# Kernel optimization log

Hardware: AMD Instinct MI355X
Metric: run time of the kernel (lower is better)

## Reference

```python
import jax, jax.numpy as jnp
import numpy as np

E = 65536
C = 128            # hidden_channels
SPH = 128          # sphere_channels
EC = 128           # edge_channels
LMAX = 3
MMAX = 2
S = 1 + 2 * LMAX   # 7
DEG_FULL = [2 * l + 1 for l in range(1, LMAX + 1)]          # [3,5,7], sum=15
DEG_RED = [min(2 * l + 1, 2 * MMAX + 1) for l in range(1, LMAX + 1)]  # [3,5,5]
D_FULL = sum(DEG_FULL)


def setup_inputs() -> dict:
    key = jax.random.key(0)
    ks = jax.random.split(key, 10)
    return {
        "attn_output": jax.random.normal(ks[0], (E, S * C), jnp.float32),
        "t_ij": jax.random.normal(ks[1], (E, EC), jnp.float32),
        "h_j": jax.random.normal(ks[2], (E, SPH), jnp.float32),
        "X_j": jax.random.normal(ks[3], (E, D_FULL, SPH), jnp.float32),
        "rl_ij": jax.random.normal(ks[4], (E, D_FULL), jnp.float32),
        # learned params
        "W_rs_w": jax.random.normal(ks[5], (S * C, EC), jnp.float32) * 0.02,
        "W_rs_b": jnp.zeros((S * C,), jnp.float32),
        "gamma_w": jax.random.normal(ks[6], (S * C, SPH), jnp.float32) * 0.02,
        "gamma_b": jnp.zeros((S * C,), jnp.float32),
        "xj_w": jax.random.normal(ks[7], (C, SPH), jnp.float32) * 0.02,
    }


def reference(attn_output, t_ij, h_j, X_j, rl_ij, W_rs_w, W_rs_b, gamma_w, gamma_b, xj_w):
    # Eq. 6: combined = attn + (t_ij W_rs) * SiLU(gamma(h_j))
    t_bias = (t_ij @ W_rs_w.T + W_rs_b) * jax.nn.silu(h_j @ gamma_w.T + gamma_b)
    combined = attn_output + t_bias              # [E, S*C]
    # split(C, dim=-1) == reshape to [E, S, C]
    o = combined.reshape(-1, S, C)
    out_scalar = jax.nn.silu(o[:, 0])[:, None, :]  # [E,1,C]
    # project neighbour features: [E, D_FULL, SPH] -> [E, D_FULL, C]
    Xp = jnp.einsum('eds,cs->edc', X_j, xj_w)
    offs = np.concatenate([[0], np.cumsum(DEG_FULL)])
    out_degrees = [out_scalar]
    for i in range(LMAX):
        m = DEG_RED[i]
        s0 = int(offs[i])
        Xl = Xp[:, s0:s0 + m, :]                  # [E, m, C]
        rl = rl_ij[:, s0:s0 + m, None]            # [E, m, 1]
        od = o[:, 1 + i][:, None, :]              # [E, 1, C]
        ot = o[:, 1 + LMAX + i][:, None, :]       # [E, 1, C]
        out_degrees.append(od * rl + ot * Xl)     # Eq. 7 per-degree
    return jnp.concatenate(out_degrees, axis=1)   # [E, 1+sum(DEG_RED), C]
```

## Files before the change

kernel.cpp:

```cpp
#include <hip/hip_runtime.h>

#define BM 64
#define KDIM 128
#define SC 896
#define LDSS 136

typedef __bf16 bf16x8 __attribute__((ext_vector_type(8)));
typedef float f32x4 __attribute__((ext_vector_type(4)));

__device__ __forceinline__ unsigned int f2bf(float f) {
  union { float f; unsigned int u; } v; v.f = f;
  unsigned int u = v.u;
  return ((u + 0x7FFFu + ((u >> 16) & 1u)) >> 16) & 0xFFFFu;
}

__device__ __forceinline__ f32x4 mfma16(uint4 a, uint4 b, f32x4 c) {
  union { uint4 u; bf16x8 v; } A, B;
  A.u = a; B.u = b;
  return __builtin_amdgcn_mfma_f32_16x16x32_bf16(A.v, B.v, c, 0, 0, 0);
}

__device__ __forceinline__ float silu_f(float x) {
  return x / (1.0f + __expf(-x));
}

__global__ void pack_kernel(const float* __restrict__ W,
                            const float* __restrict__ G,
                            const float* __restrict__ XW,
                            unsigned short* __restrict__ Wp,
                            unsigned short* __restrict__ Gp,
                            unsigned short* __restrict__ XWp) {
  int g = blockIdx.x * blockDim.x + threadIdx.x;
  const float* src;
  unsigned short* dst;
  int gg;
  if (g < 14336)       { src = W;  dst = Wp;  gg = g; }
  else if (g < 28672)  { src = G;  dst = Gp;  gg = g - 14336; }
  else                 { src = XW; dst = XWp; gg = g - 28672; }
  int lane = gg & 63;
  int kt = (gg >> 6) & 3;
  int nt = (gg >> 8) & 7;
  int J  = gg >> 11;
  int n  = J * 128 + nt * 16 + (lane & 15);
  int kb = kt * 32 + (lane >> 4) * 8;
  const float* s = src + n * 128 + kb;
  unsigned short* o = dst + gg * 8;
#pragma unroll
  for (int t = 0; t < 8; t++) o[t] = (unsigned short)f2bf(s[t]);
}

__device__ __forceinline__ void compute_o(
    int j, const unsigned short* tbase, const unsigned short* hbase,
    const uint4* __restrict__ Wp, const uint4* __restrict__ Gp,
    const float* __restrict__ b1, const float* __restrict__ b2,
    const float* __restrict__ attn, int e_r0, int ln, int lane, f32x4 o[8]) {
  const f32x4 zero = {0.f, 0.f, 0.f, 0.f};
  f32x4 g[8];
#pragma unroll
  for (int nt = 0; nt < 8; nt++) g[nt] = zero;
#pragma unroll
  for (int kt = 0; kt < 4; kt++) {
    uint4 a = *(const uint4*)(hbase + kt * 32);
#pragma unroll
    for (int nt = 0; nt < 8; nt++) {
      uint4 b = Gp[(((j * 8 + nt) * 4 + kt) << 6) + lane];
      g[nt] = mfma16(a, b, g[nt]);
    }
  }
#pragma unroll
  for (int nt = 0; nt < 8; nt++) {
    float bias = b2[j * 128 + nt * 16 + ln];
#pragma unroll
    for (int r = 0; r < 4; r++) g[nt][r] = silu_f(g[nt][r] + bias);
  }
  f32x4 acc[8];
#pragma unroll
  for (int nt = 0; nt < 8; nt++) acc[nt] = zero;
#pragma unroll
  for (int kt = 0; kt < 4; kt++) {
    uint4 a = *(const uint4*)(tbase + kt * 32);
#pragma unroll
    for (int nt = 0; nt < 8; nt++) {
      uint4 b = Wp[(((j * 8 + nt) * 4 + kt) << 6) + lane];
      acc[nt] = mfma16(a, b, acc[nt]);
    }
  }
#pragma unroll
  for (int nt = 0; nt < 8; nt++) {
    float bias = b1[j * 128 + nt * 16 + ln];
#pragma unroll
    for (int r = 0; r < 4; r++) {
      float at = attn[(e_r0 + r) * SC + j * 128 + nt * 16 + ln];
      o[nt][r] = at + (acc[nt][r] + bias) * g[nt][r];
    }
  }
}

__global__ __launch_bounds__(256, 2) void gata_main(
    const float* __restrict__ attn, const float* __restrict__ t_ij,
    const float* __restrict__ h_j, const float* __restrict__ X_j,
    const float* __restrict__ rl_ij, const float* __restrict__ b1,
    const float* __restrict__ b2, const uint4* __restrict__ Wp,
    const uint4* __restrict__ Gp, const uint4* __restrict__ XWp,
    float* __restrict__ out) {
  __shared__ __align__(16) unsigned short tA[BM * LDSS];
  __shared__ __align__(16) unsigned short hA[BM * LDSS];
  __shared__ float rlS[BM * 13];

  const int tid = threadIdx.x;
  const int lane = tid & 63;
  const int wave = tid >> 6;
  const int ln = lane & 15;
  const int quad = lane >> 4;
  const int e0 = blockIdx.x * BM;

#pragma unroll
  for (int it = 0; it < 8; it++) {
    int f4 = tid + it * 256;
    int r = f4 >> 5;
    int c4 = (f4 & 31) << 2;
    float4 tv = *(const float4*)(t_ij + (e0 + r) * KDIM + c4);
    float4 hv = *(const float4*)(h_j + (e0 + r) * KDIM + c4);
    uint2 tw, hw;
    tw.x = f2bf(tv.x) | (f2bf(tv.y) << 16);
    tw.y = f2bf(tv.z) | (f2bf(tv.w) << 16);
    hw.x = f2bf(hv.x) | (f2bf(hv.y) << 16);
    hw.y = f2bf(hv.z) | (f2bf(hv.w) << 16);
    *(uint2*)(tA + r * LDSS + c4) = tw;
    *(uint2*)(hA + r * LDSS + c4) = hw;
  }
#pragma unroll
  for (int it = 0; it < 4; it++) {
    int idx = tid + it * 256;
    if (idx < BM * 13) {
      int r = idx / 13;
      int d = idx - r * 13;
      rlS[idx] = rl_ij[(e0 + r) * 15 + d];
    }
  }
  __syncthreads();

  const int ew = e0 + wave * 16;
  const int e_r0 = ew + quad * 4;
  const unsigned short* tbase = tA + (wave * 16 + ln) * LDSS + quad * 8;
  const unsigned short* hbase = hA + (wave * 16 + ln) * LDSS + quad * 8;
  const f32x4 zero = {0.f, 0.f, 0.f, 0.f};

  {
    f32x4 o0[8];
    compute_o(0, tbase, hbase, Wp, Gp, b1, b2, attn, e_r0, ln, lane, o0);
#pragma unroll
    for (int nt = 0; nt < 8; nt++)
#pragma unroll
      for (int r = 0; r < 4; r++)
        out[((e_r0 + r) * 14 + 0) * 128 + nt * 16 + ln] = silu_f(o0[nt][r]);
  }

  const int s0s[3] = {0, 3, 8};
  const int ms[3] = {3, 5, 5};
  for (int i = 0; i < 3; i++) {
    f32x4 oA[8], oB[8];
    compute_o(1 + i, tbase, hbase, Wp, Gp, b1, b2, attn, e_r0, ln, lane, oA);
    compute_o(4 + i, tbase, hbase, Wp, Gp, b1, b2, attn, e_r0, ln, lane, oB);
    const int s0 = s0s[i];
    const int sEnd = s0 + ms[i];
    for (int d = s0; d < sEnd; d++) {
      f32x4 xp[8];
#pragma unroll
      for (int nt = 0; nt < 8; nt++) xp[nt] = zero;
      const float* xrow = X_j + ((ew + ln) * 15 + d) * KDIM + quad * 8;
#pragma unroll
      for (int kt = 0; kt < 4; kt++) {
        float4 x0 = *(const float4*)(xrow + kt * 32);
        float4 x1 = *(const float4*)(xrow + kt * 32 + 4);
        uint4 a;
        a.x = f2bf(x0.x) | (f2bf(x0.y) << 16);
        a.y = f2bf(x0.z) | (f2bf(x0.w) << 16);
        a.z = f2bf(x1.x) | (f2bf(x1.y) << 16);
        a.w = f2bf(x1.z) | (f2bf(x1.w) << 16);
#pragma unroll
        for (int nt = 0; nt < 8; nt++) {
          uint4 b = XWp[((nt * 4 + kt) << 6) + lane];
          xp[nt] = mfma16(a, b, xp[nt]);
        }
      }
#pragma unroll
      for (int r = 0; r < 4; r++) {
        float rl = rlS[(wave * 16 + quad * 4 + r) * 13 + d];
#pragma unroll
        for (int nt = 0; nt < 8; nt++) {
          float v = oA[nt][r] * rl + oB[nt][r] * xp[nt][r];
          out[((e_r0 + r) * 14 + 1 + d) * 128 + nt * 16 + ln] = v;
        }
      }
    }
  }
}

extern "C" void kernel_launch(void* const* d_in, const int* in_sizes, int n_in,
                              void* d_out, int out_size, void* d_ws, size_t ws_size,
                              hipStream_t stream) {
  const float* attn = (const float*)d_in[0];
  const float* t_ij = (const float*)d_in[1];
  const float* h_j  = (const float*)d_in[2];
  const float* X_j  = (const float*)d_in[3];
  const float* rl   = (const float*)d_in[4];
  const float* W    = (const float*)d_in[5];
  const float* b1   = (const float*)d_in[6];
  const float* G    = (const float*)d_in[7];
  const float* b2   = (const float*)d_in[8];
  const float* XW   = (const float*)d_in[9];

  unsigned short* Wp  = (unsigned short*)d_ws;
  unsigned short* Gp  = Wp + 14336 * 8;
  unsigned short* XWp = Gp + 14336 * 8;

  const int E = in_sizes[1] / KDIM;
  pack_kernel<<<120, 256, 0, stream>>>(W, G, XW, Wp, Gp, XWp);
  gata_main<<<E / BM, 256, 0, stream>>>(attn, t_ij, h_j, X_j, rl, b1, b2,
                                        (const uint4*)Wp, (const uint4*)Gp,
                                        (const uint4*)XWp, (float*)d_out);
}
```

Measured before the change: 1.372 ms.

## Permute weight columns so MFMA outputs allow vectorized attn/out access, prefetch X rows

The packed weight layout is permuted so each lane's eight N-tiles hold four consecutive output columns in each 64-column half. The attn loads, bias loads and output stores can then use 16-byte vector accesses instead of scalar strided ones. X_j rows for the next degree are also loaded one iteration ahead, so global load latency overlaps with the MFMA work. The cost is higher register pressure from the prefetch buffers under launch_bounds(256,2).

```diff
diff --git a/kernel.cpp b/kernel.cpp
--- a/kernel.cpp
+++ b/kernel.cpp
@@ -41,7 +41,7 @@
   int kt = (gg >> 6) & 3;
   int nt = (gg >> 8) & 7;
   int J  = gg >> 11;
-  int n  = J * 128 + nt * 16 + (lane & 15);
+  int n  = J * 128 + (nt >> 2) * 64 + (lane & 15) * 4 + (nt & 3);
   int kb = kt * 32 + (lane >> 4) * 8;
   const float* s = src + n * 128 + kb;
   unsigned short* o = dst + gg * 8;
@@ -55,6 +55,13 @@
     const float* __restrict__ b1, const float* __restrict__ b2,
     const float* __restrict__ attn, int e_r0, int ln, int lane, f32x4 o[8]) {
   const f32x4 zero = {0.f, 0.f, 0.f, 0.f};
+  const uint4* Gj = Gp + j * 2048 + lane;
+  const uint4* Wj = Wp + j * 2048 + lane;
+  f32x4 bg0 = *(const f32x4*)(b2 + j * 128 + ln * 4);
+  f32x4 bg1 = *(const f32x4*)(b2 + j * 128 + 64 + ln * 4);
+  f32x4 bw0 = *(const f32x4*)(b1 + j * 128 + ln * 4);
+  f32x4 bw1 = *(const f32x4*)(b1 + j * 128 + 64 + ln * 4);
+
   f32x4 g[8];
 #pragma unroll
   for (int nt = 0; nt < 8; nt++) g[nt] = zero;
@@ -62,17 +69,25 @@
   for (int kt = 0; kt < 4; kt++) {
     uint4 a = *(const uint4*)(hbase + kt * 32);
 #pragma unroll
-    for (int nt = 0; nt < 8; nt++) {
-      uint4 b = Gp[(((j * 8 + nt) * 4 + kt) << 6) + lane];
-      g[nt] = mfma16(a, b, g[nt]);
-    }
-  }
+    for (int nt = 0; nt < 8; nt++)
+      g[nt] = mfma16(a, Gj[(nt * 4 + kt) * 64], g[nt]);
+  }
+
+  f32x4 at0[4], at1[4];
+  const float* abase = attn + j * 128 + ln * 4;
+#pragma unroll
+  for (int r = 0; r < 4; r++) {
+    at0[r] = *(const f32x4*)(abase + (e_r0 + r) * SC);
+    at1[r] = *(const f32x4*)(abase + (e_r0 + r) * SC + 64);
+  }
+
 #pragma unroll
   for (int nt = 0; nt < 8; nt++) {
-    float bias = b2[j * 128 + nt * 16 + ln];
+    float bias = (nt < 4) ? bg0[nt] : bg1[nt - 4];
 #pragma unroll
     for (int r = 0; r < 4; r++) g[nt][r] = silu_f(g[nt][r] + bias);
   }
+
   f32x4 acc[8];
 #pragma unroll
   for (int nt = 0; nt < 8; nt++) acc[nt] = zero;
@@ -80,17 +95,16 @@
   for (int kt = 0; kt < 4; kt++) {
     uint4 a = *(const uint4*)(tbase + kt * 32);
 #pragma unroll
-    for (int nt = 0; nt < 8; nt++) {
-      uint4 b = Wp[(((j * 8 + nt) * 4 + kt) << 6) + lane];
-      acc[nt] = mfma16(a, b, acc[nt]);
-    }
-  }
+    for (int nt = 0; nt < 8; nt++)
+      acc[nt] = mfma16(a, Wj[(nt * 4 + kt) * 64], acc[nt]);
+  }
+
 #pragma unroll
   for (int nt = 0; nt < 8; nt++) {
-    float bias = b1[j * 128 + nt * 16 + ln];
+    float bias = (nt < 4) ? bw0[nt] : bw1[nt - 4];
 #pragma unroll
     for (int r = 0; r < 4; r++) {
-      float at = attn[(e_r0 + r) * SC + j * 128 + nt * 16 + ln];
+      float at = (nt < 4) ? at0[r][nt] : at1[r][nt - 4];
       o[nt][r] = at + (acc[nt][r] + bias) * g[nt][r];
     }
   }
@@ -144,55 +158,82 @@
   const int e_r0 = ew + quad * 4;
   const unsigned short* tbase = tA + (wave * 16 + ln) * LDSS + quad * 8;
   const unsigned short* hbase = hA + (wave * 16 + ln) * LDSS + quad * 8;
+  const uint4* XWl = XWp + lane;
   const f32x4 zero = {0.f, 0.f, 0.f, 0.f};
 
   {
     f32x4 o0[8];
     compute_o(0, tbase, hbase, Wp, Gp, b1, b2, attn, e_r0, ln, lane, o0);
 #pragma unroll
-    for (int nt = 0; nt < 8; nt++)
-#pragma unroll
-      for (int r = 0; r < 4; r++)
-        out[((e_r0 + r) * 14 + 0) * 128 + nt * 16 + ln] = silu_f(o0[nt][r]);
+    for (int r = 0; r < 4; r++) {
+      f32x4 v0, v1;
+#pragma unroll
+      for (int q = 0; q < 4; q++) {
+        v0[q] = silu_f(o0[q][r]);
+        v1[q] = silu_f(o0[4 + q][r]);
+      }
+      float* p = out + ((e_r0 + r) * 14 + 0) * 128 + ln * 4;
+      *(f32x4*)p = v0;
+      *(f32x4*)(p + 64) = v1;
+    }
   }
 
   const int s0s[3] = {0, 3, 8};
   const int ms[3] = {3, 5, 5};
+  const float* xbase = X_j + (ew + ln) * 15 * KDIM + quad * 8;
   for (int i = 0; i < 3; i++) {
     f32x4 oA[8], oB[8];
     compute_o(1 + i, tbase, hbase, Wp, Gp, b1, b2, attn, e_r0, ln, lane, oA);
     compute_o(4 + i, tbase, hbase, Wp, Gp, b1, b2, attn, e_r0, ln, lane, oB);
     const int s0 = s0s[i];
     const int sEnd = s0 + ms[i];
+
+    f32x4 xv[8];
+#pragma unroll
+    for (int kt = 0; kt < 4; kt++) {
+      xv[2 * kt]     = *(const f32x4*)(xbase + s0 * KDIM + kt * 32);
+      xv[2 * kt + 1] = *(const f32x4*)(xbase + s0 * KDIM + kt * 32 + 4);
+    }
     for (int d = s0; d < sEnd; d++) {
+      uint4 af[4];
+#pragma unroll
+      for (int kt = 0; kt < 4; kt++) {
+        af[kt].x = f2bf(xv[2 * kt][0])     | (f2bf(xv[2 * kt][1]) << 16);
+        af[kt].y = f2bf(xv[2 * kt][2])     | (f2bf(xv[2 * kt][3]) << 16);
+        af[kt].z = f2bf(xv[2 * kt + 1][0]) | (f2bf(xv[2 * kt + 1][1]) << 16);
+        af[kt].w = f2bf(xv[2 * kt + 1][2]) | (f2bf(xv[2 * kt + 1][3]) << 16);
+      }
+      int dn = (d + 1 < sEnd) ? d + 1 : d;
+      f32x4 xn[8];
+#pragma unroll
+      for (int kt = 0; kt < 4; kt++) {
+        xn[2 * kt]     = *(const f32x4*)(xbase + dn * KDIM + kt * 32);
+        xn[2 * kt + 1] = *(const f32x4*)(xbase + dn * KDIM + kt * 32 + 4);
+      }
       f32x4 xp[8];
 #pragma unroll
       for (int nt = 0; nt < 8; nt++) xp[nt] = zero;
-      const float* xrow = X_j + ((ew + ln) * 15 + d) * KDIM + quad * 8;
 #pragma unroll
       for (int kt = 0; kt < 4; kt++) {
-        float4 x0 = *(const float4*)(xrow + kt * 32);
-        float4 x1 = *(const float4*)(xrow + kt * 32 + 4);
-        uint4 a;
-        a.x = f2bf(x0.x) | (f2bf(x0.y) << 16);
-        a.y = f2bf(x0.z) | (f2bf(x0.w) << 16);
-        a.z = f2bf(x1.x) | (f2bf(x1.y) << 16);
-        a.w = f2bf(x1.z) | (f2bf(x1.w) << 16);
-#pragma unroll
-        for (int nt = 0; nt < 8; nt++) {
-          uint4 b = XWp[((nt * 4 + kt) << 6) + lane];
-          xp[nt] = mfma16(a, b, xp[nt]);
-        }
+#pragma unroll
+        for (int nt = 0; nt < 8; nt++)
+          xp[nt] = mfma16(af[kt], XWl[(nt * 4 + kt) * 64], xp[nt]);
       }
 #pragma unroll
       for (int r = 0; r < 4; r++) {
         float rl = rlS[(wave * 16 + quad * 4 + r) * 13 + d];
-#pragma unroll
-        for (int nt = 0; nt < 8; nt++) {
-          float v = oA[nt][r] * rl + oB[nt][r] * xp[nt][r];
-          out[((e_r0 + r) * 14 + 1 + d) * 128 + nt * 16 + ln] = v;
+        f32x4 v0, v1;
+#pragma unroll
+        for (int q = 0; q < 4; q++) {
+          v0[q] = oA[q][r] * rl + oB[q][r] * xp[q][r];
+          v1[q] = oA[4 + q][r] * rl + oB[4 + q][r] * xp[4 + q][r];
         }
-      }
+        float* p = out + ((e_r0 + r) * 14 + 1 + d) * 128 + ln * 4;
+        *(f32x4*)p = v0;
+        *(f32x4*)(p + 64) = v1;
+      }
+#pragma unroll
+      for (int k = 0; k < 8; k++) xv[k] = xn[k];
     }
   }
 }
```

Measured after the change: 1.181 ms. 1.16x faster.
